# Kernel optimization log

Hardware: AMD Instinct MI355X
Metric: run time of the kernel (lower is better)

## Reference

```python
import jax, jax.numpy as jnp
import numpy as np

NEG_INF = -9999.0  # same masking constant as the TF code


def avgpool3_same(x):
    """TF average_pooling1d(pool=3, stride=1, padding='SAME') on [B, L, D].
    TF avg-pool excludes padded positions from the divisor (count 2 at edges)."""
    L = x.shape[1]
    s = x
    s = s + jnp.pad(x[:, 1:], ((0, 0), (0, 1), (0, 0)))   # right neighbor
    s = s + jnp.pad(x[:, :-1], ((0, 0), (1, 0), (0, 0)))  # left neighbor
    counts = jnp.full((L,), 3.0, dtype=x.dtype).at[0].set(2.0).at[-1].set(2.0)
    return s / counts[None, :, None]


def setup_inputs() -> dict:
    key = jax.random.key(0)
    k1, k2, k3, k4 = jax.random.split(key, 4)
    B, S, T, D, Vs, Vt = 64, 128, 128, 1024, 32000, 32000
    source_sent = jax.random.randint(k1, (B, S), 0, Vs, dtype=jnp.int32)
    target_sent = jax.random.randint(k2, (B, T), 0, Vt, dtype=jnp.int32)
    # masks: mostly valid tokens with padding tails (id==0 treated as pad)
    source_mask = source_sent > 0
    target_mask = target_sent > 0
    xavier_s = (6.0 / (Vs + D)) ** 0.5
    xavier_t = (6.0 / (Vt + D)) ** 0.5
    source_emb_table = jax.random.uniform(k3, (Vs, D), jnp.float32, -xavier_s, xavier_s)
    target_emb_table = jax.random.uniform(k4, (Vt, D), jnp.float32, -xavier_t, xavier_t)
    return {
        "source_sent": source_sent,
        "target_sent": target_sent,
        "source_mask": source_mask,
        "target_mask": target_mask,
        "source_emb_table": source_emb_table,
        "target_emb_table": target_emb_table,
    }


def reference(source_sent, target_sent, source_mask, target_mask,
              source_emb_table, target_emb_table):
    # embedding lookup + avg-pool(3, SAME) residual smoothing
    src = source_emb_table[source_sent]              # [B, S, D]
    tgt = target_emb_table[target_sent]              # [B, T, D]
    src = avgpool3_same(src) + src
    tgt = avgpool3_same(tgt) + tgt

    # joint validity mask [B, S, T]
    mask = source_mask[:, :, None] & target_mask[:, None, :]

    # bidirectional alignment scores
    mul_score = jnp.einsum('btd,bsd->bts', tgt, src)  # [B, T, S]

    # target->source attention: mask^T is [B, T, S]
    ta_score = jnp.where(jnp.transpose(mask, (0, 2, 1)), mul_score, NEG_INF)
    ta_soft_score = jax.nn.softmax(ta_score, axis=-1)
    source_att_embed = jnp.einsum('bts,bsd->btd', ta_soft_score, src)  # [B, T, D]

    # source->target attention
    at_score = jnp.where(mask, jnp.transpose(mul_score, (0, 2, 1)), NEG_INF)
    at_soft_score = jax.nn.softmax(at_score, axis=-1)
    target_att_embed = jnp.einsum('bst,btd->bsd', at_soft_score, tgt)  # [B, S, D]

    return (src, source_att_embed, at_soft_score,
            tgt, target_att_embed, ta_soft_score)
```

## Files before the change

kernel.cpp:

```cpp
#include <hip/hip_runtime.h>
#include <math.h>


#define NEG_INF -9999.0f

typedef __attribute__((ext_vector_type(8))) short   bf16x8;
typedef __attribute__((ext_vector_type(4))) float   f32x4;
typedef __attribute__((ext_vector_type(8))) unsigned short u16x8;

static __device__ inline ushort f2bf(float f) {
    union { float f; unsigned u; } v; v.f = f;
    unsigned r = v.u + 0x7fff + ((v.u >> 16) & 1);
    return (ushort)(r >> 16);
}

static __device__ inline int xcd_swz(int bid, int cpx) {
    return (bid & 7) * cpx + (bid >> 3);
}

__global__ __launch_bounds__(256) void k_embed_all5(
    const int* __restrict__ ssent, const int* __restrict__ tsent,
    const float* __restrict__ stab, const float* __restrict__ ttab,
    float* __restrict__ srcO, float* __restrict__ tgtO,
    ushort* __restrict__ ebS, ushort* __restrict__ ebT)
{
    __shared__ float sm[66][136];
    int blk = blockIdx.x;
    int side = blk >> 10;
    int rem = blk & 1023;
    int b = rem >> 4;
    int p0 = ((rem >> 3) & 1) << 6;
    int d0 = (rem & 7) << 7;
    const int*   sent  = side ? tsent : ssent;
    const float* table = side ? ttab  : stab;
    float*  out = side ? tgtO : srcO;
    ushort* eb  = side ? ebT  : ebS;

    int tid = threadIdx.x;
    const int* ids = sent + b * 128;
    int pg = tid >> 5;
    int c4 = (tid & 31) << 2;

    int myids[9];
#pragma unroll
    for (int i = 0; i < 9; ++i) {
        int row = pg + (i << 3);
        int pos = p0 + row - 1;
        pos = pos < 0 ? 0 : (pos > 127 ? 127 : pos);
        myids[i] = (row < 66) ? ids[pos] : 0;
    }

#pragma unroll
    for (int i = 0; i < 9; ++i) {
        int row = pg + (i << 3);
        if (row < 66) {
            float4 v = *(const float4*)(table + (size_t)myids[i] * 1024 + d0 + c4);
            *(float4*)&sm[row][c4] = v;
        }
    }
    __syncthreads();

#pragma unroll
    for (int pp = 0; pp < 8; ++pp) {
        int pl = (pp << 3) + pg;
        int pos = p0 + pl;
        float4 c = *(const float4*)&sm[pl + 1][c4];
        float4 a = c;
        if (pos > 0) {
            float4 p = *(const float4*)&sm[pl][c4];
            a.x += p.x; a.y += p.y; a.z += p.z; a.w += p.w;
        }
        if (pos < 127) {
            float4 n = *(const float4*)&sm[pl + 2][c4];
            a.x += n.x; a.y += n.y; a.z += n.z; a.w += n.w;
        }
        float inv = (pos == 0 || pos == 127) ? 0.5f : (1.0f / 3.0f);
        float4 o;
        o.x = fmaf(a.x, inv, c.x); o.y = fmaf(a.y, inv, c.y);
        o.z = fmaf(a.z, inv, c.z); o.w = fmaf(a.w, inv, c.w);
        size_t base = (size_t)b * 131072 + (size_t)pos * 1024 + d0 + c4;
        *(float4*)(out + base) = o;
        ushort4 h;
        h.x = f2bf(o.x); h.y = f2bf(o.y); h.z = f2bf(o.z); h.w = f2bf(o.w);
        *(ushort4*)(eb + base) = h;
    }
}

__global__ __launch_bounds__(256) void k_scores_splitk(
    const ushort* __restrict__ ebS, const ushort* __restrict__ ebT,
    float* __restrict__ mul)
{
    __shared__ float red[3][64][17];
    int blk = xcd_swz(blockIdx.x, 128);
    int b = blk >> 4;
    int t0 = ((blk >> 2) & 3) * 32, s0 = (blk & 3) * 32;
    int tid = threadIdx.x;
    int w = tid >> 6, l = tid & 63;
    int rA = l & 15, kg = (l >> 4) << 3;
    int kbase = w << 8;
    const ushort* sp = ebS + (size_t)b * 131072 + (size_t)(s0 + rA) * 1024 + kbase + kg;
    const ushort* tp = ebT + (size_t)b * 131072 + (size_t)(t0 + rA) * 1024 + kbase + kg;
    f32x4 acc[2][2] = {};
#pragma unroll 4
    for (int k0 = 0; k0 < 256; k0 += 32) {
        bf16x8 sf[2], tf[2];
#pragma unroll
        for (int i = 0; i < 2; ++i) {
            sf[i] = *(const bf16x8*)(sp + (size_t)(i << 4) * 1024 + k0);
            tf[i] = *(const bf16x8*)(tp + (size_t)(i << 4) * 1024 + k0);
        }
#pragma unroll
        for (int i = 0; i < 2; ++i)
#pragma unroll
            for (int j = 0; j < 2; ++j)
                acc[i][j] = __builtin_amdgcn_mfma_f32_16x16x32_bf16(
                    sf[i], tf[j], acc[i][j], 0, 0, 0);
    }
    if (w > 0) {
#pragma unroll
        for (int i = 0; i < 2; ++i)
#pragma unroll
            for (int j = 0; j < 2; ++j)
#pragma unroll
                for (int r = 0; r < 4; ++r)
                    red[w - 1][l][((i << 1) + j) * 4 + r] = acc[i][j][r];
    }
    __syncthreads();
    if (w == 0) {
#pragma unroll
        for (int i = 0; i < 2; ++i)
#pragma unroll
            for (int j = 0; j < 2; ++j)
#pragma unroll
                for (int r = 0; r < 4; ++r) {
                    int idx = ((i << 1) + j) * 4 + r;
                    acc[i][j][r] += red[0][l][idx] + red[1][l][idx] + red[2][l][idx];
                }
        float* mb = mul + (size_t)b * 16384;
        int cn = l & 15, sq = (l >> 4) << 2;
#pragma unroll
        for (int i = 0; i < 2; ++i)
#pragma unroll
            for (int j = 0; j < 2; ++j)
                *(f32x4*)(mb + (size_t)(t0 + (j << 4) + cn) * 128
                             + s0 + (i << 4) + sq) = acc[i][j];
    }
}

__global__ __launch_bounds__(64) void k_softmax_dual(
    const float* __restrict__ mul, const int* __restrict__ ssent,
    const int* __restrict__ tsent, float* __restrict__ at,
    float* __restrict__ ta, ushort* __restrict__ pat, ushort* __restrict__ pta)
{
    int blk = xcd_swz(blockIdx.x, 1024);
    int b = blk >> 7, i = blk & 127;
    int lane = threadIdx.x;
    const float* mb = mul + (size_t)b * 16384;
    bool sv0 = ssent[b * 128 + lane] > 0, sv1 = ssent[b * 128 + lane + 64] > 0;
    bool tv0 = tsent[b * 128 + lane] > 0, tv1 = tsent[b * 128 + lane + 64] > 0;

    {
        bool tm = tsent[b * 128 + i] > 0;
        float v0 = (tm && sv0) ? mb[i * 128 + lane] : NEG_INF;
        float v1 = (tm && sv1) ? mb[i * 128 + lane + 64] : NEG_INF;
        float m = fmaxf(v0, v1);
#pragma unroll
        for (int off = 32; off; off >>= 1) m = fmaxf(m, __shfl_xor(m, off));
        float e0 = __expf(v0 - m), e1 = __expf(v1 - m);
        float sum = e0 + e1;
#pragma unroll
        for (int off = 32; off; off >>= 1) sum += __shfl_xor(sum, off);
        float r = 1.0f / sum;
        float p0 = e0 * r, p1 = e1 * r;
        size_t o = (size_t)blk * 128;
        ta[o + lane] = p0; ta[o + lane + 64] = p1;
        pta[o + lane] = f2bf(p0); pta[o + lane + 64] = f2bf(p1);
    }
    {
        bool smk = ssent[b * 128 + i] > 0;
        float v0 = (smk && tv0) ? mb[lane * 128 + i] : NEG_INF;
        float v1 = (smk && tv1) ? mb[(lane + 64) * 128 + i] : NEG_INF;
        float m = fmaxf(v0, v1);
#pragma unroll
        for (int off = 32; off; off >>= 1) m = fmaxf(m, __shfl_xor(m, off));
        float e0 = __expf(v0 - m), e1 = __expf(v1 - m);
        float sum = e0 + e1;
#pragma unroll
        for (int off = 32; off; off >>= 1) sum += __shfl_xor(sum, off);
        float r = 1.0f / sum;
        float p0 = e0 * r, p1 = e1 * r;
        size_t o = (size_t)blk * 128;
        at[o + lane] = p0; at[o + lane + 64] = p1;
        pat[o + lane] = f2bf(p0); pat[o + lane + 64] = f2bf(p1);
    }
}

__global__ __launch_bounds__(64) void k_attmm3(
    const ushort* __restrict__ pta, const ushort* __restrict__ ebS,
    float* __restrict__ satt,
    const ushort* __restrict__ pat, const ushort* __restrict__ ebT,
    float* __restrict__ tatt)
{
    __shared__ ushort ldsE[128][44];
    int blk = xcd_swz(blockIdx.x, 1024);
    int q = blk >> 12;
    int rem = blk & 4095;
    int b = rem >> 6;
    int rt = (rem >> 5) & 1, dt = rem & 31;
    const ushort* P = q ? pat : pta;
    const ushort* E = q ? ebT : ebS;
    float* C = q ? tatt : satt;
    int r0 = rt << 6, d0 = dt << 5;
    int l = threadIdx.x;

    {
        int pr = l >> 2, dd = (l & 3) << 3;
        const ushort* srcp = E + (size_t)b * 131072 + d0 + dd;
#pragma unroll
        for (int it = 0; it < 8; ++it) {
            int pos = (it << 4) + pr;
            u16x8 v = *(const u16x8*)(srcp + (size_t)pos * 1024);
            *(uint2*)&ldsE[pos][dd]     = *(const uint2*)&v;
            *(uint2*)&ldsE[pos][dd + 4] = *((const uint2*)&v + 1);
        }
    }
    __syncthreads();

    int rA = l & 15, kg = (l >> 4) << 3;
    const ushort* Pb = P + (size_t)b * 16384 + (size_t)(r0 + rA) * 128 + kg;
    f32x4 acc[4][2] = {};
#pragma unroll
    for (int k0 = 0; k0 < 128; k0 += 32) {
        bf16x8 pf[4], ef[2];
#pragma unroll
        for (int i = 0; i < 4; ++i)
            pf[i] = *(const bf16x8*)(Pb + (i << 4) * 128 + k0);
#pragma unroll
        for (int j = 0; j < 2; ++j) {
            int d = (j << 4) + rA;
#pragma unroll
            for (int kk = 0; kk < 8; ++kk)
                ef[j][kk] = (short)ldsE[k0 + kg + kk][d];
        }
#pragma unroll
        for (int i = 0; i < 4; ++i)
#pragma unroll
            for (int j = 0; j < 2; ++j)
                acc[i][j] = __builtin_amdgcn_mfma_f32_16x16x32_bf16(
                    ef[j], pf[i], acc[i][j], 0, 0, 0);
    }
    float* Cb = C + (size_t)b * 131072;
    int cn = l & 15, dq = (l >> 4) << 2;
#pragma unroll
    for (int i = 0; i < 4; ++i)
#pragma unroll
        for (int j = 0; j < 2; ++j)
            *(f32x4*)(Cb + (size_t)(r0 + (i << 4) + cn) * 1024
                         + d0 + (j << 4) + dq) = acc[i][j];
}

__global__ __launch_bounds__(256) void k_embed_pool(
    const int* __restrict__ sent, const float* __restrict__ table,
    float* __restrict__ out)
{
    int blk = blockIdx.x;
    int b = blk >> 7, pos = blk & 127;
    const int* ids = sent + b * 128;
    int idc = ids[pos];
    int idp = (pos > 0)   ? ids[pos - 1] : -1;
    int idn = (pos < 127) ? ids[pos + 1] : -1;
    float inv = (pos == 0 || pos == 127) ? 0.5f : (1.0f / 3.0f);
    int d4 = threadIdx.x;
    float4 c = ((const float4*)(table + (size_t)idc * 1024))[d4];
    float4 a = c;
    if (idp >= 0) {
        float4 p = ((const float4*)(table + (size_t)idp * 1024))[d4];
        a.x += p.x; a.y += p.y; a.z += p.z; a.w += p.w;
    }
    if (idn >= 0) {
        float4 n = ((const float4*)(table + (size_t)idn * 1024))[d4];
        a.x += n.x; a.y += n.y; a.z += n.z; a.w += n.w;
    }
    float4 o;
    o.x = fmaf(a.x, inv, c.x); o.y = fmaf(a.y, inv, c.y);
    o.z = fmaf(a.z, inv, c.z); o.w = fmaf(a.w, inv, c.w);
    ((float4*)(out + (size_t)blk * 1024))[d4] = o;
}

__global__ __launch_bounds__(256) void k_scores(
    const float* __restrict__ srcE, const float* __restrict__ tgtE,
    float* __restrict__ mul)
{
    __shared__ float At[32][68];
    __shared__ float Bs[32][68];
    int b = blockIdx.y;
    int t0 = (blockIdx.x >> 1) * 64, s0 = (blockIdx.x & 1) * 64;
    const float* tg = tgtE + (size_t)b * 131072;
    const float* sr = srcE + (size_t)b * 131072;
    int tid = threadIdx.x, ty = tid >> 4, tx = tid & 15;
    float acc[4][4] = {};
    for (int k0 = 0; k0 < 1024; k0 += 32) {
        for (int q = tid; q < 512; q += 256) {
            int r = q >> 3, kc = (q & 7) << 2;
            float4 v = *(const float4*)(tg + (size_t)(t0 + r) * 1024 + k0 + kc);
            At[kc+0][r] = v.x; At[kc+1][r] = v.y; At[kc+2][r] = v.z; At[kc+3][r] = v.w;
            float4 w2 = *(const float4*)(sr + (size_t)(s0 + r) * 1024 + k0 + kc);
            Bs[kc+0][r] = w2.x; Bs[kc+1][r] = w2.y; Bs[kc+2][r] = w2.z; Bs[kc+3][r] = w2.w;
        }
        __syncthreads();
#pragma unroll 8
        for (int kk = 0; kk < 32; ++kk) {
            float4 av = *(const float4*)&At[kk][ty << 2];
            float4 bv = *(const float4*)&Bs[kk][tx << 2];
            float aa[4] = {av.x, av.y, av.z, av.w};
            float bb[4] = {bv.x, bv.y, bv.z, bv.w};
#pragma unroll
            for (int i = 0; i < 4; ++i)
#pragma unroll
                for (int j = 0; j < 4; ++j)
                    acc[i][j] = fmaf(aa[i], bb[j], acc[i][j]);
        }
        __syncthreads();
    }
    float* mb = mul + (size_t)b * 16384;
#pragma unroll
    for (int i = 0; i < 4; ++i)
        *(float4*)(mb + (size_t)(t0 + (ty << 2) + i) * 128 + s0 + (tx << 2)) =
            make_float4(acc[i][0], acc[i][1], acc[i][2], acc[i][3]);
}

__global__ __launch_bounds__(64) void k_softmax_at(
    const float* __restrict__ mul, const int* __restrict__ ssent,
    const int* __restrict__ tsent, float* __restrict__ at)
{
    int blk = blockIdx.x;
    int b = blk >> 7, s = blk & 127;
    int lane = threadIdx.x;
    bool smk = ssent[b * 128 + s] > 0;
    const float* mb = mul + (size_t)b * 16384;
    int t0 = lane, t1 = lane + 64;
    float v0 = (smk && tsent[b * 128 + t0] > 0) ? mb[(size_t)t0 * 128 + s] : NEG_INF;
    float v1 = (smk && tsent[b * 128 + t1] > 0) ? mb[(size_t)t1 * 128 + s] : NEG_INF;
    float m = fmaxf(v0, v1);
#pragma unroll
    for (int off = 32; off; off >>= 1) m = fmaxf(m, __shfl_xor(m, off));
    float e0 = __expf(v0 - m), e1 = __expf(v1 - m);
    float sum = e0 + e1;
#pragma unroll
    for (int off = 32; off; off >>= 1) sum += __shfl_xor(sum, off);
    float r = 1.0f / sum;
    float* ab = at + (size_t)blk * 128;
    ab[t0] = e0 * r; ab[t1] = e1 * r;
}

__global__ __launch_bounds__(64) void k_softmax_ta(
    float* __restrict__ mul, const int* __restrict__ ssent,
    const int* __restrict__ tsent)
{
    int blk = blockIdx.x;
    int b = blk >> 7, t = blk & 127;
    int lane = threadIdx.x;
    bool tm = tsent[b * 128 + t] > 0;
    float* mb = mul + (size_t)blk * 128;
    int s0 = lane, s1 = lane + 64;
    float v0 = (tm && ssent[b * 128 + s0] > 0) ? mb[s0] : NEG_INF;
    float v1 = (tm && ssent[b * 128 + s1] > 0) ? mb[s1] : NEG_INF;
    float m = fmaxf(v0, v1);
#pragma unroll
    for (int off = 32; off; off >>= 1) m = fmaxf(m, __shfl_xor(m, off));
    float e0 = __expf(v0 - m), e1 = __expf(v1 - m);
    float sum = e0 + e1;
#pragma unroll
    for (int off = 32; off; off >>= 1) sum += __shfl_xor(sum, off);
    float r = 1.0f / sum;
    mb[s0] = e0 * r; mb[s1] = e1 * r;
}

__global__ __launch_bounds__(256) void k_attmm(
    const float* __restrict__ P, const float* __restrict__ E,
    float* __restrict__ C)
{
    __shared__ float Pt[32][68];
    __shared__ float Et[32][68];
    int b = blockIdx.y;
    int r0 = (blockIdx.x >> 4) * 64, d0 = (blockIdx.x & 15) * 64;
    const float* Pb = P + (size_t)b * 16384;
    const float* Eb = E + (size_t)b * 131072;
    float* Cb = C + (size_t)b * 131072;
    int tid = threadIdx.x, ty = tid >> 4, tx = tid & 15;
    float acc[4][4] = {};
    for (int k0 = 0; k0 < 128; k0 += 32) {
        for (int q = tid; q < 512; q += 256) {
            int r = q >> 3, kc = (q & 7) << 2;
            float4 v = *(const float4*)(Pb + (size_t)(r0 + r) * 128 + k0 + kc);
            Pt[kc+0][r] = v.x; Pt[kc+1][r] = v.y; Pt[kc+2][r] = v.z; Pt[kc+3][r] = v.w;
            int kr = q >> 4, dc = (q & 15) << 2;
            *(float4*)&Et[kr][dc] = *(const float4*)(Eb + (size_t)(k0 + kr) * 1024 + d0 + dc);
        }
        __syncthreads();
#pragma unroll 8
        for (int kk = 0; kk < 32; ++kk) {
            float4 av = *(const float4*)&Pt[kk][ty << 2];
            float4 bv = *(const float4*)&Et[kk][tx << 2];
            float aa[4] = {av.x, av.y, av.z, av.w};
            float bb[4] = {bv.x, bv.y, bv.z, bv.w};
#pragma unroll
            for (int i = 0; i < 4; ++i)
#pragma unroll
                for (int j = 0; j < 4; ++j)
                    acc[i][j] = fmaf(aa[i], bb[j], acc[i][j]);
        }
        __syncthreads();
    }
#pragma unroll
    for (int i = 0; i < 4; ++i)
        *(float4*)(Cb + (size_t)(r0 + (ty << 2) + i) * 1024 + d0 + (tx << 2)) =
            make_float4(acc[i][0], acc[i][1], acc[i][2], acc[i][3]);
}

extern "C" void kernel_launch(void* const* d_in, const int* in_sizes, int n_in,
                              void* d_out, int out_size, void* d_ws, size_t ws_size,
                              hipStream_t stream)
{
    const int*   ssent = (const int*)d_in[0];
    const int*   tsent = (const int*)d_in[1];
    const float* stab  = (const float*)d_in[4];
    const float* ttab  = (const float*)d_in[5];
    float* out  = (float*)d_out;

    float* src  = out + 0;
    float* satt = out + 8388608;
    float* at   = out + 16777216;
    float* tgt  = out + 17825792;
    float* tatt = out + 26214400;
    float* ta   = out + 34603008;

    const size_t EB_ELEMS = 8388608;
    const size_t P_ELEMS  = 1048576;
    const size_t WS_NEED  = (2 * EB_ELEMS + 2 * P_ELEMS) * sizeof(ushort)
                          + P_ELEMS * sizeof(float);

    if (ws_size >= WS_NEED) {
        ushort* ebS  = (ushort*)d_ws;
        ushort* ebT  = ebS  + EB_ELEMS;
        ushort* pta  = ebT  + EB_ELEMS;
        ushort* pat  = pta  + P_ELEMS;
        float*  mulraw = (float*)(pat + P_ELEMS);

        k_embed_all5<<<2048, 256, 0, stream>>>(ssent, tsent, stab, ttab,
                                               src, tgt, ebS, ebT);
        k_scores_splitk<<<1024, 256, 0, stream>>>(ebS, ebT, mulraw);
        k_softmax_dual<<<8192, 64, 0, stream>>>(mulraw, ssent, tsent,
                                                at, ta, pat, pta);
        k_attmm3<<<8192, 64, 0, stream>>>(pta, ebS, satt, pat, ebT, tatt);
    } else {
        k_embed_pool<<<8192, 256, 0, stream>>>(ssent, stab, src);
        k_embed_pool<<<8192, 256, 0, stream>>>(tsent, ttab, tgt);
        k_scores<<<dim3(4, 64), 256, 0, stream>>>(src, tgt, ta);
        k_softmax_at<<<8192, 64, 0, stream>>>(ta, ssent, tsent, at);
        k_softmax_ta<<<8192, 64, 0, stream>>>(ta, ssent, tsent);
        k_attmm<<<dim3(32, 64), 256, 0, stream>>>(ta, src, satt);
        k_attmm<<<dim3(32, 64), 256, 0, stream>>>(at, tgt, tatt);
    }
}
```

Before: 87.16 us.

## Drop bf16 embedding copies; convert fp32 outputs to bf16 inside consumer kernels

The embed kernel no longer writes separate bf16 copies of the pooled embeddings. The score and attention-matmul kernels now read the fp32 src/tgt outputs directly and convert them to bf16 in registers. This removes 32MB of bf16 writes and the workspace they used. In exchange, the consumers read twice as many bytes per element, and attmm re-reads the embeddings once per row-tile block, which may increase total read traffic.

```diff
diff --git a/kernel.cpp b/kernel.cpp
--- a/kernel.cpp
+++ b/kernel.cpp
@@ -1,4 +1,5 @@
 #include <hip/hip_runtime.h>
+#include <hip/hip_bf16.h>
 #include <math.h>
 
 
@@ -14,15 +15,27 @@
     return (ushort)(r >> 16);
 }
 
+static __device__ inline short fbs(float f) {
+    union { __hip_bfloat16 h; short s; } u;
+    u.h = __float2bfloat16(f);
+    return u.s;
+}
+
+static __device__ inline bf16x8 pack8(float4 a, float4 b) {
+    bf16x8 r;
+    r[0] = fbs(a.x); r[1] = fbs(a.y); r[2] = fbs(a.z); r[3] = fbs(a.w);
+    r[4] = fbs(b.x); r[5] = fbs(b.y); r[6] = fbs(b.z); r[7] = fbs(b.w);
+    return r;
+}
+
 static __device__ inline int xcd_swz(int bid, int cpx) {
     return (bid & 7) * cpx + (bid >> 3);
 }
 
-__global__ __launch_bounds__(256) void k_embed_all5(
+__global__ __launch_bounds__(256) void k_embed_all6(
     const int* __restrict__ ssent, const int* __restrict__ tsent,
     const float* __restrict__ stab, const float* __restrict__ ttab,
-    float* __restrict__ srcO, float* __restrict__ tgtO,
-    ushort* __restrict__ ebS, ushort* __restrict__ ebT)
+    float* __restrict__ srcO, float* __restrict__ tgtO)
 {
     __shared__ float sm[66][136];
     int blk = blockIdx.x;
@@ -33,8 +46,7 @@
     int d0 = (rem & 7) << 7;
     const int*   sent  = side ? tsent : ssent;
     const float* table = side ? ttab  : stab;
-    float*  out = side ? tgtO : srcO;
-    ushort* eb  = side ? ebT  : ebS;
+    float* out = side ? tgtO : srcO;
 
     int tid = threadIdx.x;
     const int* ids = sent + b * 128;
@@ -78,16 +90,12 @@
         float4 o;
         o.x = fmaf(a.x, inv, c.x); o.y = fmaf(a.y, inv, c.y);
         o.z = fmaf(a.z, inv, c.z); o.w = fmaf(a.w, inv, c.w);
-        size_t base = (size_t)b * 131072 + (size_t)pos * 1024 + d0 + c4;
-        *(float4*)(out + base) = o;
-        ushort4 h;
-        h.x = f2bf(o.x); h.y = f2bf(o.y); h.z = f2bf(o.z); h.w = f2bf(o.w);
-        *(ushort4*)(eb + base) = h;
-    }
-}
-
-__global__ __launch_bounds__(256) void k_scores_splitk(
-    const ushort* __restrict__ ebS, const ushort* __restrict__ ebT,
+        *(float4*)(out + (size_t)b * 131072 + (size_t)pos * 1024 + d0 + c4) = o;
+    }
+}
+
+__global__ __launch_bounds__(256) void k_scores_splitk2(
+    const float* __restrict__ srcE, const float* __restrict__ tgtE,
     float* __restrict__ mul)
 {
     __shared__ float red[3][64][17];
@@ -98,16 +106,18 @@
     int w = tid >> 6, l = tid & 63;
     int rA = l & 15, kg = (l >> 4) << 3;
     int kbase = w << 8;
-    const ushort* sp = ebS + (size_t)b * 131072 + (size_t)(s0 + rA) * 1024 + kbase + kg;
-    const ushort* tp = ebT + (size_t)b * 131072 + (size_t)(t0 + rA) * 1024 + kbase + kg;
+    const float* sp = srcE + (size_t)b * 131072 + (size_t)(s0 + rA) * 1024 + kbase + kg;
+    const float* tp = tgtE + (size_t)b * 131072 + (size_t)(t0 + rA) * 1024 + kbase + kg;
     f32x4 acc[2][2] = {};
 #pragma unroll 4
     for (int k0 = 0; k0 < 256; k0 += 32) {
         bf16x8 sf[2], tf[2];
 #pragma unroll
         for (int i = 0; i < 2; ++i) {
-            sf[i] = *(const bf16x8*)(sp + (size_t)(i << 4) * 1024 + k0);
-            tf[i] = *(const bf16x8*)(tp + (size_t)(i << 4) * 1024 + k0);
+            const float* pa = sp + (size_t)(i << 4) * 1024 + k0;
+            sf[i] = pack8(*(const float4*)pa, *(const float4*)(pa + 4));
+            const float* pb = tp + (size_t)(i << 4) * 1024 + k0;
+            tf[i] = pack8(*(const float4*)pb, *(const float4*)(pb + 4));
         }
 #pragma unroll
         for (int i = 0; i < 2; ++i)
@@ -195,10 +205,10 @@
     }
 }
 
-__global__ __launch_bounds__(64) void k_attmm3(
-    const ushort* __restrict__ pta, const ushort* __restrict__ ebS,
+__global__ __launch_bounds__(64) void k_attmm4(
+    const ushort* __restrict__ pta, const float* __restrict__ srcE,
     float* __restrict__ satt,
-    const ushort* __restrict__ pat, const ushort* __restrict__ ebT,
+    const ushort* __restrict__ pat, const float* __restrict__ tgtE,
     float* __restrict__ tatt)
 {
     __shared__ ushort ldsE[128][44];
@@ -208,20 +218,26 @@
     int b = rem >> 6;
     int rt = (rem >> 5) & 1, dt = rem & 31;
     const ushort* P = q ? pat : pta;
-    const ushort* E = q ? ebT : ebS;
+    const float* E = q ? tgtE : srcE;
     float* C = q ? tatt : satt;
     int r0 = rt << 6, d0 = dt << 5;
     int l = threadIdx.x;
 
     {
         int pr = l >> 2, dd = (l & 3) << 3;
-        const ushort* srcp = E + (size_t)b * 131072 + d0 + dd;
+        const float* srcp = E + (size_t)b * 131072 + d0 + dd;
 #pragma unroll
         for (int it = 0; it < 8; ++it) {
             int pos = (it << 4) + pr;
-            u16x8 v = *(const u16x8*)(srcp + (size_t)pos * 1024);
-            *(uint2*)&ldsE[pos][dd]     = *(const uint2*)&v;
-            *(uint2*)&ldsE[pos][dd + 4] = *((const uint2*)&v + 1);
+            float4 v0 = *(const float4*)(srcp + (size_t)pos * 1024);
+            float4 v1 = *(const float4*)(srcp + (size_t)pos * 1024 + 4);
+            u16x8 h;
+            h[0] = (ushort)fbs(v0.x); h[1] = (ushort)fbs(v0.y);
+            h[2] = (ushort)fbs(v0.z); h[3] = (ushort)fbs(v0.w);
+            h[4] = (ushort)fbs(v1.x); h[5] = (ushort)fbs(v1.y);
+            h[6] = (ushort)fbs(v1.z); h[7] = (ushort)fbs(v1.w);
+            *(uint2*)&ldsE[pos][dd]     = *(const uint2*)&h;
+            *(uint2*)&ldsE[pos][dd + 4] = *((const uint2*)&h + 1);
         }
     }
     __syncthreads();
@@ -435,24 +451,21 @@
     float* tatt = out + 26214400;
     float* ta   = out + 34603008;
 
-    const size_t EB_ELEMS = 8388608;
-    const size_t P_ELEMS  = 1048576;
-    const size_t WS_NEED  = (2 * EB_ELEMS + 2 * P_ELEMS) * sizeof(ushort)
-                          + P_ELEMS * sizeof(float);
+    const size_t P_ELEMS = 1048576;
+    const size_t WS_NEED = 2 * P_ELEMS * sizeof(ushort)
+                         + P_ELEMS * sizeof(float);
 
     if (ws_size >= WS_NEED) {
-        ushort* ebS  = (ushort*)d_ws;
-        ushort* ebT  = ebS  + EB_ELEMS;
-        ushort* pta  = ebT  + EB_ELEMS;
-        ushort* pat  = pta  + P_ELEMS;
+        ushort* pta  = (ushort*)d_ws;
+        ushort* pat  = pta + P_ELEMS;
         float*  mulraw = (float*)(pat + P_ELEMS);
 
-        k_embed_all5<<<2048, 256, 0, stream>>>(ssent, tsent, stab, ttab,
-                                               src, tgt, ebS, ebT);
-        k_scores_splitk<<<1024, 256, 0, stream>>>(ebS, ebT, mulraw);
+        k_embed_all6<<<2048, 256, 0, stream>>>(ssent, tsent, stab, ttab,
+                                               src, tgt);
+        k_scores_splitk2<<<1024, 256, 0, stream>>>(src, tgt, mulraw);
         k_softmax_dual<<<8192, 64, 0, stream>>>(mulraw, ssent, tsent,
                                                 at, ta, pat, pta);
-        k_attmm3<<<8192, 64, 0, stream>>>(pta, ebS, satt, pat, ebT, tatt);
+        k_attmm4<<<8192, 64, 0, stream>>>(pta, src, satt, pat, tgt, tatt);
     } else {
         k_embed_pool<<<8192, 256, 0, stream>>>(ssent, stab, src);
         k_embed_pool<<<8192, 256, 0, stream>>>(tsent, ttab, tgt);
```

Measured after the change: 99.67 us. 1.14x slower.
